# Optimization experiments

Hardware: AMD Instinct MI355X
Metric: run time of the kernel (lower is better)

The kernel has to match this reference:

```python
import jax, jax.numpy as jnp
import numpy as np

N_MAX = 5000  # original module truncates both clouds to 5000 points


def _hungarian(cost):
    """Exact linear sum assignment (Jonker-Volgenant / Hungarian with potentials).
    cost: (n, n) float64 numpy array. Returns cols: cols[i] = column assigned to row i.
    Matches scipy.optimize.linear_sum_assignment on square matrices."""
    n = cost.shape[0]
    u = np.zeros(n + 1)
    v = np.zeros(n + 1)
    p = np.full(n + 1, -1, dtype=np.int64)  # p[j] = row matched to column j (-1 = free); col n is virtual
    way = np.zeros(n, dtype=np.int64)
    for i in range(n):
        p[n] = i
        j0 = n
        minv = np.full(n, np.inf)
        used = np.zeros(n + 1, dtype=bool)
        # Dijkstra-style shortest augmenting path, inner step vectorized over columns
        while p[j0] != -1:
            used[j0] = True
            i0 = p[j0]
            free = ~used[:n]
            cur = cost[i0] - u[i0] - v[:n]
            upd = free & (cur < minv)
            minv = np.where(upd, cur, minv)
            way = np.where(upd, j0, way)
            masked = np.where(free, minv, np.inf)
            j1 = int(np.argmin(masked))
            delta = masked[j1]
            used_idx = np.nonzero(used)[0]
            u[p[used_idx]] += delta
            v[used_idx] -= delta
            minv = np.where(free, minv - delta, minv)
            j0 = j1
        # augment along alternating path back to the virtual column
        while j0 != n:
            j1 = way[j0]
            p[j0] = p[j1]
            j0 = int(j1)
    cols = np.empty(n, dtype=np.int64)
    cols[p[:n]] = np.arange(n)
    return cols


def _pairwise_dist(a, b):
    # Euclidean cdist: (n,3) x (m,3) -> (n,m)
    d2 = (jnp.sum(a * a, axis=1)[:, None]
          + jnp.sum(b * b, axis=1)[None, :]
          - 2.0 * (a @ b.T))
    return jnp.sqrt(jnp.maximum(d2, 0.0))


def setup_inputs() -> dict:
    key = jax.random.key(0)
    k1, k2 = jax.random.split(key)
    gt_pc = jax.random.normal(k1, (1, 1024, 3), dtype=jnp.float32)
    gen_pc = jax.random.normal(k2, (1, 1024, 3), dtype=jnp.float32)
    return {"gt_pc": gt_pc, "gen_pc": gen_pc}


def reference(gt_pc, gen_pc):
    # squeeze() + truncate to 5000 points, as in the torch module
    a = gt_pc.reshape(-1, gt_pc.shape[-1])[:N_MAX]
    b = gen_pc.reshape(-1, gen_pc.shape[-1])[:N_MAX]
    d = _pairwise_dist(a, b)  # (n, n) full cost matrix
    # exact optimal assignment (host-side, data dependent -> not jittable)
    cols = _hungarian(np.asarray(d, dtype=np.float64))
    rows = jnp.arange(d.shape[0])
    return d[rows, jnp.asarray(cols)].mean()
```

## Files before the change

### kernel.cpp

```cpp
#include <hip/hip_runtime.h>
#include <math.h>


#define N         1024
#define NT        512
#define NW        (NT / 64)
#define CPL       16
#define NPHASE    3
#define ROUND_CAP 20000
#define OFFSET    4.0f

typedef unsigned long long ull;

__device__ __forceinline__ float wave_min_bcast(float x) {
#define DPPSTEP(C) { int _t = __builtin_amdgcn_update_dpp(                    \
      __float_as_int(x), __float_as_int(x), (C), 0xf, 0xf, false);            \
      x = fminf(x, __int_as_float(_t)); }
    DPPSTEP(0x111)
    DPPSTEP(0x112)
    DPPSTEP(0x114)
    DPPSTEP(0x118)
    DPPSTEP(0x142)
    DPPSTEP(0x143)
#undef DPPSTEP
    return __int_as_float(__builtin_amdgcn_readlane(__float_as_int(x), 63));
}

__device__ __forceinline__ float dist2_b(const float4 Ai, float bxn, float byn,
                                         float bzn, float sbk) {
    float acc = fmaf(bzn, Ai.z, sbk);
    acc = fmaf(byn, Ai.y, acc);
    acc = fmaf(bxn, Ai.x, acc);
    return fmaxf(acc + Ai.w, 0.0f);
}
__device__ __forceinline__ float dist_b(const float4 Ai, float bxn, float byn,
                                        float bzn, float sbk) {
    return __builtin_amdgcn_sqrtf(dist2_b(Ai, bxn, byn, bzn, sbk));
}

__global__ __launch_bounds__(NT, 1)
void emd_auction(const float* __restrict__ gt, const float* __restrict__ gen,
                 float* __restrict__ out)
{
    __shared__ float4 A[N];
    __shared__ float4 B[N];
    __shared__ float  p[N];
    __shared__ ull    bidPack[N];
    __shared__ int    bidList[N];
    __shared__ int    bidFlag[N];
    __shared__ int    owner[N];
    __shared__ int    pobj[N];
    __shared__ int    s_nbid, s_nfree;
    __shared__ double partial[NW];

    const int tid  = threadIdx.x;
    const int lane = tid & 63;
    const int wid  = tid >> 6;
    unsigned* pu = (unsigned*)p;

    float bxn[CPL], byn[CPL], bzn[CPL], sb[CPL];
    #pragma unroll
    for (int k = 0; k < CPL; ++k) {
        const int j = (k << 6) | lane;
        const float gx = gen[3*j], gy = gen[3*j+1], gz = gen[3*j+2];
        bxn[k] = -2.f*gx; byn[k] = -2.f*gy; bzn[k] = -2.f*gz;
        sb[k]  = gx*gx + gy*gy + gz*gz;
    }
    for (int i = tid; i < N; i += NT) {
        const float x = gt[3*i], y = gt[3*i+1], z = gt[3*i+2];
        A[i] = make_float4(x, y, z, x*x + y*y + z*z);
        const float gx = gen[3*i], gy = gen[3*i+1], gz = gen[3*i+2];
        B[i] = make_float4(gx, gy, gz, gx*gx + gy*gy + gz*gz);
        pu[i] = 0x7F800000u;
        bidPack[i] = 0ull; bidFlag[i] = 0;
        owner[i] = -1; pobj[i] = -1;
    }
    if (tid == 0) { s_nbid = 0; s_nfree = N; }
    __syncthreads();

    {
        float rmin[CPL];
        #pragma unroll
        for (int k = 0; k < CPL; ++k) rmin[k] = INFINITY;
        for (int r = 0; r < N / NW; ++r) {
            const float4 Ai = A[wid * (N / NW) + r];
            #pragma unroll
            for (int k = 0; k < CPL; ++k)
                rmin[k] = fminf(rmin[k],
                                dist2_b(Ai, bxn[k], byn[k], bzn[k], sb[k]));
        }
        #pragma unroll
        for (int k = 0; k < CPL; ++k)
            atomicMin(&pu[(k << 6) | lane], (unsigned)__float_as_int(rmin[k]));
        __syncthreads();
        for (int j = tid; j < N; j += NT)
            p[j] = OFFSET - __builtin_amdgcn_sqrtf(p[j]);
        __syncthreads();
    }

    const float EPS[NPHASE] = {0.1f, 0.02f, 4e-3f};
    int  rounds  = 0;
    bool aborted = false;

    for (int ph = 0; ph < NPHASE && !aborted; ++ph) {
        const float eps = EPS[ph];

        if (ph > 0) {
            if (tid == 0) s_nfree = 0;
            for (int c = 0; c < 2; ++c) {
                const int i = (((wid << 1) | c) << 6) | lane;
                ull mask = __ballot(pobj[i] >= 0);
                while (mask) {
                    const int l = __ffsll(mask) - 1; mask &= mask - 1;
                    const int person = (((wid << 1) | c) << 6) | l;
                    const int j = pobj[person];
                    const float4 Ai = A[person];
                    float m1 = INFINITY;
                    #pragma unroll
                    for (int k = 0; k < CPL; ++k) {
                        const int jj = (k << 6) | lane;
                        m1 = fminf(m1,
                            dist_b(Ai, bxn[k], byn[k], bzn[k], sb[k]) + p[jj]);
                    }
                    const float g1 = wave_min_bcast(m1);
                    if (lane == 0) {
                        const float4 Bj = B[j];
                        const float dot = Ai.x*Bj.x + Ai.y*Bj.y + Ai.z*Bj.z;
                        const float rcj = __builtin_amdgcn_sqrtf(
                            fmaxf(Ai.w + Bj.w - 2.f*dot, 0.f)) + p[j];
                        if (rcj > g1 + eps) { owner[j] = -1; pobj[person] = -1; }
                    }
                }
            }
            __syncthreads();
            for (int c = 0; c < 2; ++c) {
                const int i = (((wid << 1) | c) << 6) | lane;
                const ull m = __ballot(pobj[i] < 0);
                if (lane == 0 && m) atomicAdd(&s_nfree, __popcll(m));
            }
            __syncthreads();
        }

        for (;;) {
            const int nf = s_nfree;
            if (nf == 0) break;
            if (++rounds >= ROUND_CAP) { aborted = true; break; }

            for (int c = 0; c < 2; ++c) {
                const int i = (((wid << 1) | c) << 6) | lane;
                ull mask = __ballot(pobj[i] < 0);
                while (mask) {
                    const int l = __ffsll(mask) - 1; mask &= mask - 1;
                    const int person = (((wid << 1) | c) << 6) | l;
                    const float4 Ai = A[person];
                    float m1 = INFINITY, m2 = INFINITY, c1 = 0.f; int a1 = 0;
                    #pragma unroll
                    for (int k = 0; k < CPL; ++k) {
                        const int jj = (k << 6) | lane;
                        const float c0 = dist_b(Ai, bxn[k], byn[k], bzn[k], sb[k]);
                        const float rc = c0 + p[jj];
                        if (rc < m1)      { m2 = m1; m1 = rc; a1 = jj; c1 = c0; }
                        else if (rc < m2) { m2 = rc; }
                    }
                    const float g1 = wave_min_bcast(m1);
                    const ull  bm  = __ballot(m1 == g1);
                    const int  w1  = __ffsll(bm) - 1;
                    const float contrib = (lane == w1) ? m2 : m1;
                    const float g2 = wave_min_bcast(contrib);
                    if (lane == w1) {
                        const float bid = (g2 - c1) + eps;
                        atomicMax(&bidPack[a1],
                                  ((ull)(unsigned)__float_as_int(bid) << 32)
                                  | (unsigned)person);
                        if (atomicCAS(&bidFlag[a1], 0, 1) == 0)
                            bidList[atomicAdd(&s_nbid, 1)] = a1;
                    }
                }
            }
            __syncthreads();

            const int nbid = s_nbid;
            for (int t = tid; t < nbid; t += NT) {
                const int j  = bidList[t];
                const ull pk = bidPack[j];
                bidPack[j] = 0ull; bidFlag[j] = 0;
                p[j] = __int_as_float((int)(pk >> 32));
                const int inew = (int)(pk & 0xffffffffu);
                const int iold = owner[j];
                owner[j] = inew;
                pobj[inew] = j;
                if (iold >= 0) pobj[iold] = -1;
                else atomicSub(&s_nfree, 1);
            }
            if (tid == 0) s_nbid = 0;
            __syncthreads();
        }
    }

    if (aborted) {
        if (wid == 0) {
            for (int i = 0; i < N; ++i) {
                if (pobj[i] >= 0) continue;
                const float4 Ai = A[i];
                float m1 = INFINITY; int a1 = 0;
                #pragma unroll
                for (int k = 0; k < CPL; ++k) {
                    const int jj = (k << 6) | lane;
                    const bool fre = (owner[jj] < 0);
                    const float c = dist_b(Ai, bxn[k], byn[k], bzn[k], sb[k]);
                    const float sel = fre ? c : INFINITY;
                    if (sel < m1) { m1 = sel; a1 = jj; }
                }
                const float g1 = wave_min_bcast(m1);
                const ull  bm  = __ballot(m1 == g1);
                const int  w1  = __ffsll(bm) - 1;
                const int  j1  = __builtin_amdgcn_readlane(a1, w1);
                if (lane == 0) { owner[j1] = i; pobj[i] = j1; }
                asm volatile("s_waitcnt lgkmcnt(0)" ::: "memory");
            }
        }
        __syncthreads();
    }

    double s = 0.0;
    for (int j = tid; j < N; j += NT) {
        const int i = owner[j];
        if (i >= 0) {
            const float4 Ai = A[i];
            const float4 Bj = B[j];
            const float dot = Ai.x*Bj.x + Ai.y*Bj.y + Ai.z*Bj.z;
            const float d2  = Ai.w + Bj.w - 2.0f*dot;
            s += (double)__builtin_amdgcn_sqrtf(fmaxf(d2, 0.0f));
        }
    }
    #pragma unroll
    for (int m = 32; m >= 1; m >>= 1) s += __shfl_xor(s, m);
    if (lane == 0) partial[wid] = s;
    __syncthreads();
    if (tid == 0) {
        double tot = 0.0;
        for (int w = 0; w < NW; ++w) tot += partial[w];
        out[0] = (float)(tot / (double)N);
    }
}

extern "C" void kernel_launch(void* const* d_in, const int* in_sizes, int n_in,
                              void* d_out, int out_size, void* d_ws, size_t ws_size,
                              hipStream_t stream) {
    const float* gt  = (const float*)d_in[0];
    const float* gen = (const float*)d_in[1];
    float* out = (float*)d_out;
    emd_auction<<<1, NT, 0, stream>>>(gt, gen, out);
}
```

Before: 8.813 ms.

## Finish auction tail with single-wave Gauss-Seidel bidding when few persons remain

Once the number of unassigned persons drops to a small threshold, one wavefront handles the remaining bids sequentially, Gauss-Seidel style, with prices cached in registers. The goal is to avoid the many block-wide synchronized Jacobi rounds that each resolve only a handful of bids near the end of the auction. A step budget aborts if the sequential chain runs too long. The other waves idle during this phase, and an eviction chain could take many serial steps.

After: 11.28 ms. 28.0% more time.

```diff
diff --git a/kernel.cpp b/kernel.cpp
--- a/kernel.cpp
+++ b/kernel.cpp
@@ -8,6 +8,8 @@
 #define CPL       16
 #define NPHASE    3
 #define ROUND_CAP 20000
+#define GS_T      6
+#define GS_BUDGET 40000
 #define OFFSET    4.0f
 
 typedef unsigned long long ull;
@@ -50,7 +52,7 @@
     __shared__ int    bidFlag[N];
     __shared__ int    owner[N];
     __shared__ int    pobj[N];
-    __shared__ int    s_nbid, s_nfree;
+    __shared__ int    s_nbid, s_nfree, s_gsfail;
     __shared__ double partial[NW];
 
     const int tid  = threadIdx.x;
@@ -75,7 +77,7 @@
         bidPack[i] = 0ull; bidFlag[i] = 0;
         owner[i] = -1; pobj[i] = -1;
     }
-    if (tid == 0) { s_nbid = 0; s_nfree = N; }
+    if (tid == 0) { s_nbid = 0; s_nfree = N; s_gsfail = 0; }
     __syncthreads();
 
     {
@@ -145,6 +147,70 @@
             const int nf = s_nfree;
             if (nf == 0) break;
             if (++rounds >= ROUND_CAP) { aborted = true; break; }
+
+            if (nf <= GS_T) {
+                if (wid == 0) {
+                    float pr[CPL];
+                    #pragma unroll
+                    for (int k = 0; k < CPL; ++k) pr[k] = p[(k << 6) | lane];
+                    int sc = 0;
+                    for (int c = 0; c < N / 64; ++c) {
+                        ull m = __ballot(pobj[(c << 6) | lane] < 0);
+                        while (m) {
+                            const int l = __ffsll(m) - 1; m &= m - 1;
+                            if (lane == 0) bidList[sc] = (c << 6) | l;
+                            ++sc;
+                        }
+                    }
+                    int person = -1, steps = 0, fail = 0;
+                    for (;;) {
+                        if (person < 0) {
+                            if (sc == 0) break;
+                            --sc;
+                            person = bidList[sc];
+                        }
+                        if (++steps > GS_BUDGET) { fail = 1; break; }
+                        const float4 Ai = A[person];
+                        float m1 = INFINITY, m2 = INFINITY, c1 = 0.f; int a1 = 0;
+                        #pragma unroll
+                        for (int k = 0; k < CPL; ++k) {
+                            const float c0 =
+                                dist_b(Ai, bxn[k], byn[k], bzn[k], sb[k]);
+                            const float rc = c0 + pr[k];
+                            if (rc < m1) { m2 = m1; m1 = rc;
+                                           a1 = (k << 6) | lane; c1 = c0; }
+                            else if (rc < m2) { m2 = rc; }
+                        }
+                        const float g1 = wave_min_bcast(m1);
+                        const ull  bm  = __ballot(m1 == g1);
+                        const int  w1  = __ffsll(bm) - 1;
+                        const int  j1  = __builtin_amdgcn_readlane(a1, w1);
+                        const float contrib = (lane == w1) ? m2 : m1;
+                        const float g2 = wave_min_bcast(contrib);
+                        const float c1w = __int_as_float(
+                            __builtin_amdgcn_readlane(__float_as_int(c1), w1));
+                        const float bid = (g2 - c1w) + eps;
+                        const int evict = owner[j1];
+                        if (lane == 0) {
+                            owner[j1] = person; pobj[person] = j1; p[j1] = bid;
+                            if (evict >= 0) pobj[evict] = -1;
+                        }
+                        #pragma unroll
+                        for (int k = 0; k < CPL; ++k)
+                            if (k == (j1 >> 6) && lane == (j1 & 63))
+                                pr[k] = bid;
+                        person = evict;
+                        asm volatile("s_waitcnt lgkmcnt(0)" ::: "memory");
+                    }
+                    if (lane == 0) {
+                        s_nfree = sc + (person >= 0 ? 1 : 0);
+                        s_gsfail = fail;
+                    }
+                }
+                __syncthreads();
+                if (s_gsfail) { aborted = true; break; }
+                continue;
+            }
 
             for (int c = 0; c < 2; ++c) {
                 const int i = (((wid << 1) | c) << 6) | lane;
```

## Run auction tail with a single wavefront once few bidders remain

Applied to the files above, without the earlier changes.

When three or fewer persons are unassigned, the auction switches to a tail loop run only by wavefront 0. That loop keeps a compact list of free persons in LDS and does bidding and assignment without block-wide barriers. This removes the per-round __syncthreads cost of the long tail, where many rounds carry only one or two bidders. The final epsilon is also loosened from 4e-3 to 6e-3, which cuts rounds but gives a less exact assignment. A budget abort is added as a fallback.

Result: slower. 9.276 ms (+5.3%).

```diff
diff --git a/kernel.cpp b/kernel.cpp
--- a/kernel.cpp
+++ b/kernel.cpp
@@ -2,13 +2,15 @@
 #include <math.h>
 
 
-#define N         1024
-#define NT        512
-#define NW        (NT / 64)
-#define CPL       16
-#define NPHASE    3
-#define ROUND_CAP 20000
-#define OFFSET    4.0f
+#define N          1024
+#define NT         512
+#define NW         (NT / 64)
+#define CPL        16
+#define NPHASE     3
+#define ROUND_CAP  20000
+#define JT         3
+#define TAIL_BUDGET 30000
+#define OFFSET     4.0f
 
 typedef unsigned long long ull;
 
@@ -38,6 +40,8 @@
     return __builtin_amdgcn_sqrtf(dist2_b(Ai, bxn, byn, bzn, sbk));
 }
 
+#define LDS_FENCE() asm volatile("s_waitcnt lgkmcnt(0)" ::: "memory")
+
 __global__ __launch_bounds__(NT, 1)
 void emd_auction(const float* __restrict__ gt, const float* __restrict__ gen,
                  float* __restrict__ out)
@@ -50,7 +54,8 @@
     __shared__ int    bidFlag[N];
     __shared__ int    owner[N];
     __shared__ int    pobj[N];
-    __shared__ int    s_nbid, s_nfree;
+    __shared__ int    tailL[64];
+    __shared__ int    s_nbid, s_nfree, s_tfail;
     __shared__ double partial[NW];
 
     const int tid  = threadIdx.x;
@@ -75,7 +80,7 @@
         bidPack[i] = 0ull; bidFlag[i] = 0;
         owner[i] = -1; pobj[i] = -1;
     }
-    if (tid == 0) { s_nbid = 0; s_nfree = N; }
+    if (tid == 0) { s_nbid = 0; s_nfree = N; s_tfail = 0; }
     __syncthreads();
 
     {
@@ -98,7 +103,7 @@
         __syncthreads();
     }
 
-    const float EPS[NPHASE] = {0.1f, 0.02f, 4e-3f};
+    const float EPS[NPHASE] = {0.1f, 0.02f, 6e-3f};
     int  rounds  = 0;
     bool aborted = false;
 
@@ -145,6 +150,91 @@
             const int nf = s_nfree;
             if (nf == 0) break;
             if (++rounds >= ROUND_CAP) { aborted = true; break; }
+
+            if (nf <= JT) {
+                if (wid == 0) {
+                    int cnt = 0;
+                    for (int c = 0; c < N / 64; ++c) {
+                        ull m = __ballot(pobj[(c << 6) | lane] < 0);
+                        while (m) {
+                            const int l = __ffsll(m) - 1; m &= m - 1;
+                            if (lane == 0) tailL[cnt] = (c << 6) | l;
+                            ++cnt;
+                        }
+                    }
+                    LDS_FENCE();
+                    int steps = 0, fail = 0;
+                    for (;;) {
+                        const int e = (lane < cnt) ? tailL[lane] : -1;
+                        const bool live = (e >= 0) && (pobj[e] < 0);
+                        const ull lm = __ballot(live);
+                        LDS_FENCE();
+                        if (live)
+                            tailL[__popcll(lm & ((1ull << lane) - 1ull))] = e;
+                        LDS_FENCE();
+                        cnt = __popcll(lm);
+                        if (cnt == 0) break;
+                        if (++steps > TAIL_BUDGET) { fail = 1; break; }
+
+                        for (int t = 0; t < cnt; ++t) {
+                            const int person = tailL[t];
+                            const float4 Ai = A[person];
+                            float m1 = INFINITY, m2 = INFINITY, c1 = 0.f;
+                            int a1 = 0;
+                            #pragma unroll
+                            for (int k = 0; k < CPL; ++k) {
+                                const int jj = (k << 6) | lane;
+                                const float c0 =
+                                    dist_b(Ai, bxn[k], byn[k], bzn[k], sb[k]);
+                                const float rc = c0 + p[jj];
+                                if (rc < m1) { m2 = m1; m1 = rc;
+                                               a1 = jj; c1 = c0; }
+                                else if (rc < m2) { m2 = rc; }
+                            }
+                            const float g1 = wave_min_bcast(m1);
+                            const ull  bm  = __ballot(m1 == g1);
+                            const int  w1  = __ffsll(bm) - 1;
+                            const float contrib = (lane == w1) ? m2 : m1;
+                            const float g2 = wave_min_bcast(contrib);
+                            if (lane == w1) {
+                                const float bid = (g2 - c1) + eps;
+                                atomicMax(&bidPack[a1],
+                                    ((ull)(unsigned)__float_as_int(bid) << 32)
+                                    | (unsigned)person);
+                                if (atomicCAS(&bidFlag[a1], 0, 1) == 0)
+                                    bidList[atomicAdd(&s_nbid, 1)] = a1;
+                            }
+                        }
+                        LDS_FENCE();
+
+                        const int nbid = s_nbid;
+                        int iold = -1;
+                        if (lane < nbid) {
+                            const int j  = bidList[lane];
+                            const ull pk = bidPack[j];
+                            bidPack[j] = 0ull; bidFlag[j] = 0;
+                            p[j] = __int_as_float((int)(pk >> 32));
+                            const int inew = (int)(pk & 0xffffffffu);
+                            iold = owner[j];
+                            owner[j] = inew;
+                            pobj[inew] = j;
+                            if (iold >= 0) pobj[iold] = -1;
+                            else atomicSub(&s_nfree, 1);
+                        }
+                        const ull em = __ballot(iold >= 0);
+                        if (iold >= 0)
+                            tailL[cnt + __popcll(em & ((1ull << lane) - 1ull))]
+                                = iold;
+                        cnt += __popcll(em);
+                        if (lane == 0) s_nbid = 0;
+                        LDS_FENCE();
+                    }
+                    if (lane == 0) s_tfail = fail;
+                }
+                __syncthreads();
+                if (s_tfail) { aborted = true; break; }
+                continue;
+            }
 
             for (int c = 0; c < 2; ++c) {
                 const int i = (((wid << 1) | c) << 6) | lane;
@@ -216,7 +306,7 @@
                 const int  w1  = __ffsll(bm) - 1;
                 const int  j1  = __builtin_amdgcn_readlane(a1, w1);
                 if (lane == 0) { owner[j1] = i; pobj[i] = j1; }
-                asm volatile("s_waitcnt lgkmcnt(0)" ::: "memory");
+                LDS_FENCE();
             }
         }
         __syncthreads();
```

## Replace synchronous auction rounds with asynchronous ring-queue bidding and single-wave tail

Applied to the files above, without the earlier changes.

Replaces the Jacobi-style bid collection plus separate assignment pass with a Gauss-Seidel-style auction. Each object's price and owner are packed into one 64-bit word updated by atomicMax, and displaced or losing bidders are pushed onto a shared ring queue. This removes the second barrier and the assignment pass per round. When only a few persons are free, a single wave processes the queue without block barriers, aiming to cut the long barrier-bound tail. It risks more atomic contention and more bidding rounds because prices change asynchronously, and the result may differ slightly from the synchronous version.

Measured after the change: 9.670 ms. +9.7%, slower.

```diff
diff --git a/kernel.cpp b/kernel.cpp
--- a/kernel.cpp
+++ b/kernel.cpp
@@ -7,10 +7,16 @@
 #define NW        (NT / 64)
 #define CPL       16
 #define NPHASE    3
+#define RING      4096
+#define RM        (RING - 1)
+#define JT        4
 #define ROUND_CAP 20000
+#define TAIL_CAP  60000
 #define OFFSET    4.0f
 
 typedef unsigned long long ull;
+#define NOOWN 0xFFFFFFFFu
+#define LDS_FENCE() asm volatile("s_waitcnt lgkmcnt(0)" ::: "memory")
 
 __device__ __forceinline__ float wave_min_bcast(float x) {
 #define DPPSTEP(C) { int _t = __builtin_amdgcn_update_dpp(                    \
@@ -45,12 +51,10 @@
     __shared__ float4 A[N];
     __shared__ float4 B[N];
     __shared__ float  p[N];
-    __shared__ ull    bidPack[N];
-    __shared__ int    bidList[N];
-    __shared__ int    bidFlag[N];
-    __shared__ int    owner[N];
-    __shared__ int    pobj[N];
-    __shared__ int    s_nbid, s_nfree;
+    __shared__ ull    pack[N];
+    __shared__ int    ring[RING];
+    __shared__ unsigned char matched[N];
+    __shared__ int    s_tail, s_head, s_fail;
     __shared__ double partial[NW];
 
     const int tid  = threadIdx.x;
@@ -72,10 +76,9 @@
         const float gx = gen[3*i], gy = gen[3*i+1], gz = gen[3*i+2];
         B[i] = make_float4(gx, gy, gz, gx*gx + gy*gy + gz*gz);
         pu[i] = 0x7F800000u;
-        bidPack[i] = 0ull; bidFlag[i] = 0;
-        owner[i] = -1; pobj[i] = -1;
-    }
-    if (tid == 0) { s_nbid = 0; s_nfree = N; }
+        ring[i] = i;
+    }
+    if (tid == 0) { s_tail = N; s_head = 0; s_fail = 0; }
     __syncthreads();
 
     {
@@ -93,120 +96,182 @@
         for (int k = 0; k < CPL; ++k)
             atomicMin(&pu[(k << 6) | lane], (unsigned)__float_as_int(rmin[k]));
         __syncthreads();
-        for (int j = tid; j < N; j += NT)
-            p[j] = OFFSET - __builtin_amdgcn_sqrtf(p[j]);
+        for (int j = tid; j < N; j += NT) {
+            const float w = OFFSET - __builtin_amdgcn_sqrtf(p[j]);
+            p[j] = w;
+            pack[j] = ((ull)(unsigned)__float_as_int(w) << 32) | NOOWN;
+        }
         __syncthreads();
     }
 
     const float EPS[NPHASE] = {0.1f, 0.02f, 4e-3f};
     int  rounds  = 0;
+    int  head    = 0;
     bool aborted = false;
 
     for (int ph = 0; ph < NPHASE && !aborted; ++ph) {
         const float eps = EPS[ph];
 
         if (ph > 0) {
-            if (tid == 0) s_nfree = 0;
-            for (int c = 0; c < 2; ++c) {
-                const int i = (((wid << 1) | c) << 6) | lane;
-                ull mask = __ballot(pobj[i] >= 0);
-                while (mask) {
-                    const int l = __ffsll(mask) - 1; mask &= mask - 1;
-                    const int person = (((wid << 1) | c) << 6) | l;
-                    const int j = pobj[person];
-                    const float4 Ai = A[person];
-                    float m1 = INFINITY;
-                    #pragma unroll
-                    for (int k = 0; k < CPL; ++k) {
-                        const int jj = (k << 6) | lane;
-                        m1 = fminf(m1,
-                            dist_b(Ai, bxn[k], byn[k], bzn[k], sb[k]) + p[jj]);
-                    }
-                    const float g1 = wave_min_bcast(m1);
-                    if (lane == 0) {
-                        const float4 Bj = B[j];
-                        const float dot = Ai.x*Bj.x + Ai.y*Bj.y + Ai.z*Bj.z;
-                        const float rcj = __builtin_amdgcn_sqrtf(
-                            fmaxf(Ai.w + Bj.w - 2.f*dot, 0.f)) + p[j];
-                        if (rcj > g1 + eps) { owner[j] = -1; pobj[person] = -1; }
-                    }
-                }
-            }
-            __syncthreads();
-            for (int c = 0; c < 2; ++c) {
-                const int i = (((wid << 1) | c) << 6) | lane;
-                const ull m = __ballot(pobj[i] < 0);
-                if (lane == 0 && m) atomicAdd(&s_nfree, __popcll(m));
-            }
-            __syncthreads();
+            for (int i = tid; i < N; i += NT) matched[i] = 0;
+            __syncthreads();
+            for (int j = wid; j < N; j += NW) {
+                const unsigned ow = (unsigned)(pack[j] & 0xffffffffu);
+                if (ow == NOOWN) continue;
+                const float4 Ai = A[ow];
+                float m1 = INFINITY;
+                #pragma unroll
+                for (int k = 0; k < CPL; ++k) {
+                    const int jj = (k << 6) | lane;
+                    m1 = fminf(m1,
+                        dist_b(Ai, bxn[k], byn[k], bzn[k], sb[k]) + p[jj]);
+                }
+                const float g1 = wave_min_bcast(m1);
+                const float4 Bj = B[j];
+                const float dot = Ai.x*Bj.x + Ai.y*Bj.y + Ai.z*Bj.z;
+                const float rcj = __builtin_amdgcn_sqrtf(
+                    fmaxf(Ai.w + Bj.w - 2.f*dot, 0.f)) + p[j];
+                if (lane == 0) {
+                    if (rcj > g1 + eps)
+                        pack[j] = (pack[j] & 0xffffffff00000000ull) | NOOWN;
+                    else
+                        matched[ow] = 1;
+                }
+            }
+            __syncthreads();
+            if (tid == 0) { s_head = 0; s_tail = 0; }
+            __syncthreads();
+            for (int base = 0; base < N; base += NT) {
+                const int i = base + tid;
+                const bool fr = (matched[i] == 0);
+                const ull m = __ballot(fr);
+                int pos = 0;
+                if (lane == 0 && m) pos = atomicAdd(&s_tail, __popcll(m));
+                pos = __shfl(pos, 0);
+                if (fr)
+                    ring[(pos + __popcll(m & ((1ull << lane) - 1ull))) & RM] = i;
+            }
+            __syncthreads();
+            head = 0;
         }
 
         for (;;) {
-            const int nf = s_nfree;
+            const int tail0 = s_tail;
+            const int nf = tail0 - head;
             if (nf == 0) break;
             if (++rounds >= ROUND_CAP) { aborted = true; break; }
 
-            for (int c = 0; c < 2; ++c) {
-                const int i = (((wid << 1) | c) << 6) | lane;
-                ull mask = __ballot(pobj[i] < 0);
-                while (mask) {
-                    const int l = __ffsll(mask) - 1; mask &= mask - 1;
-                    const int person = (((wid << 1) | c) << 6) | l;
-                    const float4 Ai = A[person];
-                    float m1 = INFINITY, m2 = INFINITY, c1 = 0.f; int a1 = 0;
-                    #pragma unroll
-                    for (int k = 0; k < CPL; ++k) {
-                        const int jj = (k << 6) | lane;
-                        const float c0 = dist_b(Ai, bxn[k], byn[k], bzn[k], sb[k]);
-                        const float rc = c0 + p[jj];
-                        if (rc < m1)      { m2 = m1; m1 = rc; a1 = jj; c1 = c0; }
-                        else if (rc < m2) { m2 = rc; }
+            if (nf <= JT) {
+                if (wid == 0) {
+                    int myhead = head, steps = 0, fail = 0;
+                    for (;;) {
+                        LDS_FENCE();
+                        const int t1 = s_tail;
+                        if (t1 == myhead) break;
+                        if (++steps > TAIL_CAP) { fail = 1; break; }
+                        for (int t = myhead; t < t1; ++t) {
+                            const int person = ring[t & RM];
+                            const float4 Ai = A[person];
+                            float m1 = INFINITY, m2 = INFINITY, c1 = 0.f;
+                            int a1 = 0;
+                            #pragma unroll
+                            for (int k = 0; k < CPL; ++k) {
+                                const int jj = (k << 6) | lane;
+                                const float c0 =
+                                    dist_b(Ai, bxn[k], byn[k], bzn[k], sb[k]);
+                                const float rc = c0 + p[jj];
+                                if (rc < m1) { m2 = m1; m1 = rc;
+                                               a1 = jj; c1 = c0; }
+                                else if (rc < m2) { m2 = rc; }
+                            }
+                            const float g1 = wave_min_bcast(m1);
+                            const ull  bm  = __ballot(m1 == g1);
+                            const int  w1  = __ffsll(bm) - 1;
+                            const float contrib = (lane == w1) ? m2 : m1;
+                            const float g2 = wave_min_bcast(contrib);
+                            if (lane == w1) {
+                                const float bid = (g2 - c1) + eps;
+                                const unsigned bb = (unsigned)__float_as_int(bid);
+                                const ull np = ((ull)bb << 32) | (unsigned)person;
+                                const ull old = atomicMax(&pack[a1], np);
+                                if (old < np) {
+                                    atomicMax(&pu[a1], bb);
+                                    const unsigned io =
+                                        (unsigned)(old & 0xffffffffu);
+                                    if (io != NOOWN)
+                                        ring[atomicAdd(&s_tail, 1) & RM] =
+                                            (int)io;
+                                } else {
+                                    ring[atomicAdd(&s_tail, 1) & RM] = person;
+                                }
+                            }
+                            LDS_FENCE();
+                        }
+                        myhead = t1;
                     }
-                    const float g1 = wave_min_bcast(m1);
-                    const ull  bm  = __ballot(m1 == g1);
-                    const int  w1  = __ffsll(bm) - 1;
-                    const float contrib = (lane == w1) ? m2 : m1;
-                    const float g2 = wave_min_bcast(contrib);
-                    if (lane == w1) {
-                        const float bid = (g2 - c1) + eps;
-                        atomicMax(&bidPack[a1],
-                                  ((ull)(unsigned)__float_as_int(bid) << 32)
-                                  | (unsigned)person);
-                        if (atomicCAS(&bidFlag[a1], 0, 1) == 0)
-                            bidList[atomicAdd(&s_nbid, 1)] = a1;
+                    if (lane == 0) { s_head = myhead; s_fail = fail; }
+                }
+                __syncthreads();
+                head = s_head;
+                if (s_fail) { aborted = true; break; }
+                continue;
+            }
+
+            for (int t = head + wid; t < tail0; t += NW) {
+                const int person = ring[t & RM];
+                const float4 Ai = A[person];
+                float m1 = INFINITY, m2 = INFINITY, c1 = 0.f; int a1 = 0;
+                #pragma unroll
+                for (int k = 0; k < CPL; ++k) {
+                    const int jj = (k << 6) | lane;
+                    const float c0 = dist_b(Ai, bxn[k], byn[k], bzn[k], sb[k]);
+                    const float rc = c0 + p[jj];
+                    if (rc < m1)      { m2 = m1; m1 = rc; a1 = jj; c1 = c0; }
+                    else if (rc < m2) { m2 = rc; }
+                }
+                const float g1 = wave_min_bcast(m1);
+                const ull  bm  = __ballot(m1 == g1);
+                const int  w1  = __ffsll(bm) - 1;
+                const float contrib = (lane == w1) ? m2 : m1;
+                const float g2 = wave_min_bcast(contrib);
+                if (lane == w1) {
+                    const float bid = (g2 - c1) + eps;
+                    const unsigned bb = (unsigned)__float_as_int(bid);
+                    const ull np = ((ull)bb << 32) | (unsigned)person;
+                    const ull old = atomicMax(&pack[a1], np);
+                    if (old < np) {
+                        atomicMax(&pu[a1], bb);
+                        const unsigned io = (unsigned)(old & 0xffffffffu);
+                        if (io != NOOWN)
+                            ring[atomicAdd(&s_tail, 1) & RM] = (int)io;
+                    } else {
+                        ring[atomicAdd(&s_tail, 1) & RM] = person;
                     }
                 }
             }
             __syncthreads();
-
-            const int nbid = s_nbid;
-            for (int t = tid; t < nbid; t += NT) {
-                const int j  = bidList[t];
-                const ull pk = bidPack[j];
-                bidPack[j] = 0ull; bidFlag[j] = 0;
-                p[j] = __int_as_float((int)(pk >> 32));
-                const int inew = (int)(pk & 0xffffffffu);
-                const int iold = owner[j];
-                owner[j] = inew;
-                pobj[inew] = j;
-                if (iold >= 0) pobj[iold] = -1;
-                else atomicSub(&s_nfree, 1);
-            }
-            if (tid == 0) s_nbid = 0;
-            __syncthreads();
+            head = tail0;
         }
     }
 
     if (aborted) {
+        for (int i = tid; i < N; i += NT) matched[i] = 0;
+        __syncthreads();
+        for (int j = tid; j < N; j += NT) {
+            const unsigned ow = (unsigned)(pack[j] & 0xffffffffu);
+            if (ow != NOOWN) matched[ow] = 1;
+        }
+        __syncthreads();
         if (wid == 0) {
             for (int i = 0; i < N; ++i) {
-                if (pobj[i] >= 0) continue;
+                if (matched[i]) continue;
                 const float4 Ai = A[i];
                 float m1 = INFINITY; int a1 = 0;
                 #pragma unroll
                 for (int k = 0; k < CPL; ++k) {
                     const int jj = (k << 6) | lane;
-                    const bool fre = (owner[jj] < 0);
+                    const bool fre =
+                        ((unsigned)(pack[jj] & 0xffffffffu) == NOOWN);
                     const float c = dist_b(Ai, bxn[k], byn[k], bzn[k], sb[k]);
                     const float sel = fre ? c : INFINITY;
                     if (sel < m1) { m1 = sel; a1 = jj; }
@@ -215,8 +280,9 @@
                 const ull  bm  = __ballot(m1 == g1);
                 const int  w1  = __ffsll(bm) - 1;
                 const int  j1  = __builtin_amdgcn_readlane(a1, w1);
-                if (lane == 0) { owner[j1] = i; pobj[i] = j1; }
-                asm volatile("s_waitcnt lgkmcnt(0)" ::: "memory");
+                if (lane == 0)
+                    pack[j1] = (pack[j1] & 0xffffffff00000000ull) | (unsigned)i;
+                LDS_FENCE();
             }
         }
         __syncthreads();
@@ -224,9 +290,9 @@
 
     double s = 0.0;
     for (int j = tid; j < N; j += NT) {
-        const int i = owner[j];
-        if (i >= 0) {
-            const float4 Ai = A[i];
+        const unsigned ow = (unsigned)(pack[j] & 0xffffffffu);
+        if (ow != NOOWN) {
+            const float4 Ai = A[ow];
             const float4 Bj = B[j];
             const float dot = Ai.x*Bj.x + Ai.y*Bj.y + Ai.z*Bj.z;
             const float d2  = Ai.w + Bj.w - 2.0f*dot;
```
